# Optimization experiments

Hardware: AMD Instinct MI355X
Metric: run time of the kernel (lower is better)

The kernel has to match this reference:

```python
import jax, jax.numpy as jnp
import numpy as np

N_NODES = 10000
N_EDGES = 160000
NUM_FEAT = 14
DIM = 256


def gat_conv(x, src, dst, W, a_s, a_d, b, concat):
    """PyG GATConv: W [H*C, F_in], a_s/a_d [H, C], edges src->dst (self-loops included)."""
    H, C = a_s.shape
    N = x.shape[0]
    h = (x @ W.T).reshape(N, H, C)                       # [N,H,C]
    alpha_src = (h * a_s).sum(-1)                        # [N,H]
    alpha_dst = (h * a_d).sum(-1)                        # [N,H]
    e = jax.nn.leaky_relu(alpha_src[src] + alpha_dst[dst], negative_slope=0.2)  # [E,H]
    emax = jax.ops.segment_max(e, dst, num_segments=N)   # [N,H]
    emax = jnp.where(jnp.isneginf(emax), 0.0, emax)
    ex = jnp.exp(e - emax[dst])
    denom = jax.ops.segment_sum(ex, dst, num_segments=N)
    coef = ex / (denom[dst] + 1e-16)                     # segment softmax over in-edges
    out = jax.ops.segment_sum(h[src] * coef[..., None], dst, num_segments=N)  # [N,H,C]
    out = out.reshape(N, H * C) if concat else out.mean(axis=1)
    return out + b


def setup_inputs() -> dict:
    key = jax.random.key(0)
    ks = jax.random.split(key, 24)
    d = DIM
    f = NUM_FEAT
    def w(k, shape, fan_in):
        return jax.random.normal(k, shape, dtype=jnp.float32) * (1.0 / np.sqrt(fan_in))
    inp = {
        "x": jax.random.normal(ks[0], (N_NODES, f), dtype=jnp.float32),
        "edge_index": jax.random.randint(ks[1], (2, N_EDGES), 0, N_NODES, dtype=jnp.int64
                                         if jax.config.jax_enable_x64 else jnp.int32),
        # conv1: 14 -> 4 heads x 256
        "W1": w(ks[2], (4 * d, f), f),
        "a1s": w(ks[3], (4, d), d), "a1d": w(ks[4], (4, d), d),
        "b1": jnp.zeros((4 * d,), jnp.float32),
        "lw1": w(ks[5], (4 * d, f), f), "lb1": jnp.zeros((4 * d,), jnp.float32),
        # conv2: 1024 -> 4 heads x 256
        "W2": w(ks[6], (4 * d, 4 * d), 4 * d),
        "a2s": w(ks[7], (4, d), d), "a2d": w(ks[8], (4, d), d),
        "b2": jnp.zeros((4 * d,), jnp.float32),
        "lw2": w(ks[9], (4 * d, 4 * d), 4 * d), "lb2": jnp.zeros((4 * d,), jnp.float32),
        # conv3: 1024 -> 6 heads x 256, mean over heads
        "W3": w(ks[10], (6 * d, 4 * d), 4 * d),
        "a3s": w(ks[11], (6, d), d), "a3d": w(ks[12], (6, d), d),
        "b3": jnp.zeros((d,), jnp.float32),
        "lw3": w(ks[13], (d, 4 * d), 4 * d), "lb3": jnp.zeros((d,), jnp.float32),
    }
    return inp


def reference(x, edge_index, W1, a1s, a1d, b1, lw1, lb1,
              W2, a2s, a2d, b2, lw2, lb2,
              W3, a3s, a3d, b3, lw3, lb3):
    N = x.shape[0]
    loops = jnp.arange(N, dtype=edge_index.dtype)
    src = jnp.concatenate([edge_index[0], loops])
    dst = jnp.concatenate([edge_index[1], loops])
    x1 = jax.nn.elu(gat_conv(x, src, dst, W1, a1s, a1d, b1, True) + x @ lw1.T + lb1)
    x2 = jax.nn.elu(gat_conv(x1, src, dst, W2, a2s, a2d, b2, True) + x1 @ lw2.T + lb2)
    x3 = gat_conv(x2, src, dst, W3, a3s, a3d, b3, False) + x2 @ lw3.T + lb3
    return x3
```

## Files before the change

kernel.cpp:

```cpp
#include <hip/hip_runtime.h>
#include <hip/hip_bf16.h>
#include <cstddef>

#define NN 10000
#define EE0 160000
#define NF 14
#define DC 256

static inline int ceildiv(int a, int b) { return (a + b - 1) / b; }

__device__ __forceinline__ float lrelu02(float x) { return fmaxf(x, 0.2f * x); }

__device__ __forceinline__ short f2bf(float f) {
    unsigned u = __float_as_uint(f);
    unsigned r = (u + 0x7FFFu + ((u >> 16) & 1u)) >> 16;
    return (short)r;
}
__device__ __forceinline__ float bf2f(short s) {
    return __uint_as_float(((unsigned)(unsigned short)s) << 16);
}

typedef __attribute__((ext_vector_type(8))) short bf16x8;
typedef __attribute__((ext_vector_type(4))) float f32x4;

#define GLDS(gaddr, laddr)                                                         \
    __builtin_amdgcn_global_load_lds(                                              \
        (__attribute__((address_space(1))) void*)(gaddr),                          \
        (__attribute__((address_space(3))) void*)(laddr), 16, 0, 0)

__global__ void count_edges_k(const int* __restrict__ ei, int* __restrict__ counts,
                              int E0, int N) {
    int e = blockIdx.x * 256 + threadIdx.x;
    int E = E0 + N;
    if (e >= E) return;
    int dst = (e < E0) ? ei[E0 + e] : (e - E0);
    atomicAdd(&counts[dst], 1);
}

__global__ __launch_bounds__(1024) void scan_k(const int* __restrict__ counts,
                                               int* __restrict__ row_off, int n) {
    __shared__ int sums[1024];
    int t = threadIdx.x;
    int chunk = (n + 1023) >> 10;
    int base = t * chunk;
    int lim = base + chunk; if (lim > n) lim = n;
    int s = 0;
    for (int i = base; i < lim; ++i) s += counts[i];
    sums[t] = s;
    __syncthreads();
    for (int off = 1; off < 1024; off <<= 1) {
        int v = (t >= off) ? sums[t - off] : 0;
        __syncthreads();
        sums[t] += v;
        __syncthreads();
    }
    int run = (t == 0) ? 0 : sums[t - 1];
    for (int i = base; i < lim; ++i) { run += counts[i]; row_off[i + 1] = run; }
    if (t == 0) row_off[0] = 0;
}

__global__ void scatter_k(const int* __restrict__ ei, const int* __restrict__ row_off,
                          int* __restrict__ cursor, int* __restrict__ csr_src,
                          int E0, int N) {
    int e = blockIdx.x * 256 + threadIdx.x;
    int E = E0 + N;
    if (e >= E) return;
    int src, dst;
    if (e < E0) { src = ei[e]; dst = ei[E0 + e]; }
    else        { src = dst = e - E0; }
    int pos = row_off[dst] + atomicAdd(&cursor[dst], 1);
    csr_src[pos] = src;
}

__global__ __launch_bounds__(256) void cvt_bf16_fused_k(
    const float* __restrict__ p0, short* __restrict__ q0, int n0,
    const float* __restrict__ p1, short* __restrict__ q1, int n1,
    const float* __restrict__ p2, short* __restrict__ q2, int n2,
    const float* __restrict__ p3, short* __restrict__ q3, int n3) {
    int i = blockIdx.x * 256 + threadIdx.x;
    const float* in; short* out; int idx;
    if (i < n0) { in = p0; out = q0; idx = i; }
    else if (i < n0 + n1) { in = p1; out = q1; idx = i - n0; }
    else if (i < n0 + n1 + n2) { in = p2; out = q2; idx = i - n0 - n1; }
    else if (i < n0 + n1 + n2 + n3) { in = p3; out = q3; idx = i - n0 - n1 - n2; }
    else return;
    float4 v = ((const float4*)in)[idx];
    short4 o;
    o.x = f2bf(v.x); o.y = f2bf(v.y); o.z = f2bf(v.z); o.w = f2bf(v.w);
    ((short4*)out)[idx] = o;
}

__global__ __launch_bounds__(256) void pad_bf16_k(
    const float* __restrict__ p0, short* __restrict__ q0, int r0,
    const float* __restrict__ p1, short* __restrict__ q1, int r1,
    const float* __restrict__ p2, short* __restrict__ q2, int r2,
    int K, int Kp) {
    int i = blockIdx.x * 256 + threadIdx.x;
    int rows = r0 + r1 + r2;
    int total = rows * Kp;
    if (i >= total) return;
    int row = i / Kp, col = i - row * Kp;
    const float* in; short* out; int r;
    if (row < r0) { in = p0; out = q0; r = row; }
    else if (row < r0 + r1) { in = p1; out = q1; r = row - r0; }
    else { in = p2; out = q2; r = row - r0 - r1; }
    out[(size_t)r * Kp + col] = (col < K) ? f2bf(in[(size_t)r * K + col]) : (short)0;
}

__global__ __launch_bounds__(256) void gemm_bf16_dual(
    const short* __restrict__ A, const short* __restrict__ B,
    const float* __restrict__ b1, const float* __restrict__ b2,
    short* __restrict__ Cb, float* __restrict__ Cf,
    int M, int Nh, int Nf, int K) {
    __shared__ short As[128 * 32];
    __shared__ short Bs[128 * 32];
    const int t = threadIdx.x;
    const int wave = t >> 6, lane = t & 63;
    const int m0 = blockIdx.y * 128, n0 = blockIdx.x * 128;
    const int wm = (wave >> 1) * 64, wn = (wave & 1) * 64;
    const int lane15 = lane & 15, quad = lane >> 4;

    const int lrow = lane >> 2;
    const int lk = ((lane & 3) ^ ((lrow >> 1) & 3)) * 8;
    int arow0 = m0 + wave * 16 + lrow;
    int arow1 = arow0 + 64;
    if (arow0 > M - 1) arow0 = M - 1;
    if (arow1 > M - 1) arow1 = M - 1;
    const short* ag0 = A + (size_t)arow0 * K + lk;
    const short* ag1 = A + (size_t)arow1 * K + lk;
    const short* bg0 = B + (size_t)(n0 + wave * 16 + lrow) * K + lk;
    const short* bg1 = B + (size_t)(n0 + 64 + wave * 16 + lrow) * K + lk;
    short* al0 = &As[(wave * 16) * 32];
    short* al1 = &As[(64 + wave * 16) * 32];
    short* bl0 = &Bs[(wave * 16) * 32];
    short* bl1 = &Bs[(64 + wave * 16) * 32];

    const int rql = (quad ^ ((lane15 >> 1) & 3)) * 8;

    f32x4 acc[4][4];
#pragma unroll
    for (int i = 0; i < 4; ++i)
#pragma unroll
        for (int j = 0; j < 4; ++j) acc[i][j] = (f32x4){0.f, 0.f, 0.f, 0.f};

    for (int k0 = 0; k0 < K; k0 += 32) {
        GLDS(ag0 + k0, al0);
        GLDS(ag1 + k0, al1);
        GLDS(bg0 + k0, bl0);
        GLDS(bg1 + k0, bl1);
        __syncthreads();
        bf16x8 af[4], bfr[4];
#pragma unroll
        for (int i = 0; i < 4; ++i)
            af[i] = *(const bf16x8*)&As[(wm + 16 * i + lane15) * 32 + rql];
#pragma unroll
        for (int j = 0; j < 4; ++j)
            bfr[j] = *(const bf16x8*)&Bs[(wn + 16 * j + lane15) * 32 + rql];
#pragma unroll
        for (int i = 0; i < 4; ++i)
#pragma unroll
            for (int j = 0; j < 4; ++j)
                acc[i][j] = __builtin_amdgcn_mfma_f32_16x16x32_bf16(
                    af[i], bfr[j], acc[i][j], 0, 0, 0);
        __syncthreads();
    }

    if (n0 >= Nh) {
#pragma unroll
        for (int j = 0; j < 4; ++j) {
            int nc = n0 - Nh + wn + 16 * j + lane15;
            float bias = b1[nc] + b2[nc];
#pragma unroll
            for (int i = 0; i < 4; ++i) {
                int mb = m0 + wm + 16 * i + quad * 4;
#pragma unroll
                for (int r = 0; r < 4; ++r) {
                    int m = mb + r;
                    if (m < M) Cf[(size_t)m * Nf + nc] = acc[i][j][r] + bias;
                }
            }
        }
    } else {
#pragma unroll
        for (int j = 0; j < 4; ++j) {
            int n = n0 + wn + 16 * j + lane15;
#pragma unroll
            for (int i = 0; i < 4; ++i) {
                int mb = m0 + wm + 16 * i + quad * 4;
#pragma unroll
                for (int r = 0; r < 4; ++r) {
                    int m = mb + r;
                    if (m < M) Cb[(size_t)m * Nh + n] = f2bf(acc[i][j][r]);
                }
            }
        }
    }
}

__global__ __launch_bounds__(256) void alpha_k(
    const short* __restrict__ h, const float* __restrict__ a_s,
    const float* __restrict__ a_d, float* __restrict__ asrc,
    float* __restrict__ adst, int N, int H) {
    int wid = (int)((blockIdx.x * (size_t)blockDim.x + threadIdx.x) >> 6);
    int lane = threadIdx.x & 63;
    if (wid >= N * H) return;
    int n = wid / H, hh = wid - n * H;
    const short4 hv4 = *(const short4*)(h + (size_t)n * H * DC + hh * DC + lane * 4);
    const float4 sv = *(const float4*)(a_s + hh * DC + lane * 4);
    const float4 dv = *(const float4*)(a_d + hh * DC + lane * 4);
    float hx = bf2f(hv4.x), hy = bf2f(hv4.y), hz = bf2f(hv4.z), hw = bf2f(hv4.w);
    float s = hx * sv.x + hy * sv.y + hz * sv.z + hw * sv.w;
    float d = hx * dv.x + hy * dv.y + hz * dv.z + hw * dv.w;
#pragma unroll
    for (int off = 32; off > 0; off >>= 1) {
        s += __shfl_down(s, off);
        d += __shfl_down(d, off);
    }
    if (lane == 0) { asrc[wid] = s; adst[wid] = d; }
}

__global__ __launch_bounds__(256) void gat_agg(
    const short* __restrict__ hbuf, const float* __restrict__ lin,
    const float* __restrict__ asrc, const float* __restrict__ adst_a,
    const int* __restrict__ row_off, const int* __restrict__ csr_src,
    short* __restrict__ outx, int N, int H) {
    int wid = (int)((blockIdx.x * (size_t)blockDim.x + threadIdx.x) >> 6);
    int lane = threadIdx.x & 63;
    if (wid >= N * H) return;
    int n = wid / H, hh = wid - n * H;
    int beg = row_off[n], end = row_off[n + 1];
    int deg = end - beg;
    float ad = adst_a[wid];

    size_t cbase = (size_t)n * H * DC + hh * DC + lane * 4;
    float4 acc = *(const float4*)(lin + cbase);

    if (deg <= 64) {
        int s = 0; float e = -1e38f;
        if (lane < deg) {
            s = csr_src[beg + lane];
            e = lrelu02(asrc[s * H + hh] + ad);
        }
        float m = e;
#pragma unroll
        for (int off = 32; off > 0; off >>= 1) m = fmaxf(m, __shfl_xor(m, off));
        float p = (lane < deg) ? __expf(e - m) : 0.f;
        float dsum = p;
#pragma unroll
        for (int off = 32; off > 0; off >>= 1) dsum += __shfl_xor(dsum, off);
        float coef = p / (dsum + 1e-16f);

        const size_t hoff = (size_t)hh * DC + lane * 4;
        int i = 0;
        for (; i + 8 <= deg; i += 8) {
            short4 v[8]; float wv[8];
#pragma unroll
            for (int u = 0; u < 8; ++u) {
                int su = __shfl(s, i + u);
                v[u] = *(const short4*)(hbuf + (size_t)su * (H * DC) + hoff);
                wv[u] = __shfl(coef, i + u);
            }
#pragma unroll
            for (int u = 0; u < 8; ++u) {
                acc.x += wv[u] * bf2f(v[u].x);
                acc.y += wv[u] * bf2f(v[u].y);
                acc.z += wv[u] * bf2f(v[u].z);
                acc.w += wv[u] * bf2f(v[u].w);
            }
        }
        for (; i < deg; ++i) {
            float wv = __shfl(coef, i);
            int si = __shfl(s, i);
            const short4 hv = *(const short4*)(hbuf + (size_t)si * (H * DC) + hoff);
            acc.x += wv * bf2f(hv.x); acc.y += wv * bf2f(hv.y);
            acc.z += wv * bf2f(hv.z); acc.w += wv * bf2f(hv.w);
        }
    } else {
        float m = -1e38f;
        for (int i = beg + lane; i < end; i += 64) {
            int s = csr_src[i];
            m = fmaxf(m, lrelu02(asrc[s * H + hh] + ad));
        }
#pragma unroll
        for (int off = 32; off > 0; off >>= 1) m = fmaxf(m, __shfl_xor(m, off));
        float dsum = 0.f;
        for (int i = beg + lane; i < end; i += 64) {
            int s = csr_src[i];
            dsum += __expf(lrelu02(asrc[s * H + hh] + ad) - m);
        }
#pragma unroll
        for (int off = 32; off > 0; off >>= 1) dsum += __shfl_xor(dsum, off);
        float inv = 1.f / (dsum + 1e-16f);
        for (int i = beg; i < end; ++i) {
            int s = csr_src[i];
            float wv = __expf(lrelu02(asrc[s * H + hh] + ad) - m) * inv;
            const short4 hv = *(const short4*)(hbuf + ((size_t)s * H + hh) * DC + lane * 4);
            acc.x += wv * bf2f(hv.x); acc.y += wv * bf2f(hv.y);
            acc.z += wv * bf2f(hv.z); acc.w += wv * bf2f(hv.w);
        }
    }
    acc.x = acc.x > 0.f ? acc.x : __expf(acc.x) - 1.f;
    acc.y = acc.y > 0.f ? acc.y : __expf(acc.y) - 1.f;
    acc.z = acc.z > 0.f ? acc.z : __expf(acc.z) - 1.f;
    acc.w = acc.w > 0.f ? acc.w : __expf(acc.w) - 1.f;
    short4 o;
    o.x = f2bf(acc.x); o.y = f2bf(acc.y); o.z = f2bf(acc.z); o.w = f2bf(acc.w);
    *(short4*)(outx + cbase) = o;
}

__global__ __launch_bounds__(384) void gat_agg_mean(
    const short* __restrict__ hbuf, const float* __restrict__ asrc,
    const float* __restrict__ adst_a, const int* __restrict__ row_off,
    const int* __restrict__ csr_src, float* __restrict__ out, int N) {
    const int H = 6;
    __shared__ float red[6][DC];
    int n = blockIdx.x;
    int wave = threadIdx.x >> 6, lane = threadIdx.x & 63;
    int hh = wave;
    int beg = row_off[n], end = row_off[n + 1];
    int deg = end - beg;
    const float invH = 1.f / 6.f;
    float ad = adst_a[n * H + hh];

    float4 acc = make_float4(0.f, 0.f, 0.f, 0.f);
    const size_t hoff = (size_t)hh * DC + lane * 4;

    if (deg <= 64) {
        int s = 0; float e = -1e38f;
        if (lane < deg) {
            s = csr_src[beg + lane];
            e = lrelu02(asrc[s * H + hh] + ad);
        }
        float m = e;
#pragma unroll
        for (int off = 32; off > 0; off >>= 1) m = fmaxf(m, __shfl_xor(m, off));
        float p = (lane < deg) ? __expf(e - m) : 0.f;
        float dsum = p;
#pragma unroll
        for (int off = 32; off > 0; off >>= 1) dsum += __shfl_xor(dsum, off);
        float coef = p * invH / (dsum + 1e-16f);

        int i = 0;
        for (; i + 8 <= deg; i += 8) {
            short4 v[8]; float wv[8];
#pragma unroll
            for (int u = 0; u < 8; ++u) {
                int su = __shfl(s, i + u);
                v[u] = *(const short4*)(hbuf + (size_t)su * (H * DC) + hoff);
                wv[u] = __shfl(coef, i + u);
            }
#pragma unroll
            for (int u = 0; u < 8; ++u) {
                acc.x += wv[u] * bf2f(v[u].x);
                acc.y += wv[u] * bf2f(v[u].y);
                acc.z += wv[u] * bf2f(v[u].z);
                acc.w += wv[u] * bf2f(v[u].w);
            }
        }
        for (; i < deg; ++i) {
            float wv = __shfl(coef, i);
            int si = __shfl(s, i);
            const short4 hv = *(const short4*)(hbuf + (size_t)si * (H * DC) + hoff);
            acc.x += wv * bf2f(hv.x); acc.y += wv * bf2f(hv.y);
            acc.z += wv * bf2f(hv.z); acc.w += wv * bf2f(hv.w);
        }
    } else {
        float m = -1e38f;
        for (int i = beg + lane; i < end; i += 64) {
            int s = csr_src[i];
            m = fmaxf(m, lrelu02(asrc[s * H + hh] + ad));
        }
#pragma unroll
        for (int off = 32; off > 0; off >>= 1) m = fmaxf(m, __shfl_xor(m, off));
        float dsum = 0.f;
        for (int i = beg + lane; i < end; i += 64) {
            int s = csr_src[i];
            dsum += __expf(lrelu02(asrc[s * H + hh] + ad) - m);
        }
#pragma unroll
        for (int off = 32; off > 0; off >>= 1) dsum += __shfl_xor(dsum, off);
        float inv = invH / (dsum + 1e-16f);
        for (int i = beg; i < end; ++i) {
            int s = csr_src[i];
            float wv = __expf(lrelu02(asrc[s * H + hh] + ad) - m) * inv;
            const short4 hv = *(const short4*)(hbuf + (size_t)s * (H * DC) + hoff);
            acc.x += wv * bf2f(hv.x); acc.y += wv * bf2f(hv.y);
            acc.z += wv * bf2f(hv.z); acc.w += wv * bf2f(hv.w);
        }
    }
    *(float4*)&red[wave][lane * 4] = acc;
    __syncthreads();
    if (wave == 0) {
        float* op = out + (size_t)n * DC + lane * 4;
        float4 o = *(float4*)op;
#pragma unroll
        for (int j = 0; j < 6; ++j) {
            float4 r = *(float4*)&red[j][lane * 4];
            o.x += r.x; o.y += r.y; o.z += r.z; o.w += r.w;
        }
        *(float4*)op = o;
    }
}

extern "C" void kernel_launch(void* const* d_in, const int* in_sizes, int n_in,
                              void* d_out, int out_size, void* d_ws, size_t ws_size,
                              hipStream_t stream) {
    const float* x   = (const float*)d_in[0];
    const int*   ei  = (const int*)d_in[1];
    const float* W1  = (const float*)d_in[2];
    const float* a1s = (const float*)d_in[3];
    const float* a1d = (const float*)d_in[4];
    const float* b1  = (const float*)d_in[5];
    const float* lw1 = (const float*)d_in[6];
    const float* lb1 = (const float*)d_in[7];
    const float* W2  = (const float*)d_in[8];
    const float* a2s = (const float*)d_in[9];
    const float* a2d = (const float*)d_in[10];
    const float* b2  = (const float*)d_in[11];
    const float* lb2_w = (const float*)d_in[12];
    const float* lb2 = (const float*)d_in[13];
    const float* W3  = (const float*)d_in[14];
    const float* a3s = (const float*)d_in[15];
    const float* a3d = (const float*)d_in[16];
    const float* b3  = (const float*)d_in[17];
    const float* lw3 = (const float*)d_in[18];
    const float* lb3 = (const float*)d_in[19];
    const float* lw2 = lb2_w;
    float* out = (float*)d_out;

    const int N = NN, E0 = EE0, E = EE0 + NN;

    unsigned char* w = (unsigned char*)d_ws;
    size_t off = 0;
    auto alloc = [&](size_t bytes) {
        void* p = w + off;
        off += (bytes + 255) & ~(size_t)255;
        return p;
    };
    short* hbuf   = (short*)alloc((size_t)N * 1536 * 2);
    float* buf    = (float*)alloc((size_t)N * 1024 * 4);
    short* xb     = (short*)alloc((size_t)N * 1024 * 2);
    short* xpad   = (short*)alloc((size_t)N * 32 * 2);
    short* W1p    = (short*)alloc((size_t)1024 * 32 * 2);
    short* lw1p   = (short*)alloc((size_t)1024 * 32 * 2);
    short* W2b    = (short*)alloc((size_t)1024 * 1024 * 2);
    short* lw2b   = (short*)alloc((size_t)1024 * 1024 * 2);
    short* W3b    = (short*)alloc((size_t)1536 * 1024 * 2);
    short* lw3b   = (short*)alloc((size_t)256 * 1024 * 2);
    float* asrc   = (float*)alloc((size_t)N * 6 * 4);
    float* adst   = (float*)alloc((size_t)N * 6 * 4);
    int* row_off  = (int*)alloc((size_t)(N + 1) * 4);
    int* counts2  = (int*)alloc((size_t)2 * N * 4);
    int* counts   = counts2;
    int* cursor   = counts2 + N;
    int* csr_src  = (int*)alloc((size_t)E * 4);
    (void)ws_size; (void)n_in; (void)in_sizes; (void)out_size;

    hipMemsetAsync(counts2, 0, (size_t)2 * N * 4, stream);
    count_edges_k<<<ceildiv(E, 256), 256, 0, stream>>>(ei, counts, E0, N);
    scan_k<<<1, 1024, 0, stream>>>(counts, row_off, N);
    scatter_k<<<ceildiv(E, 256), 256, 0, stream>>>(ei, row_off, cursor, csr_src, E0, N);

    {
        int q0 = 1024 * 1024 / 4, q1 = 1024 * 1024 / 4, q2 = 1536 * 1024 / 4,
            q3 = 256 * 1024 / 4;
        cvt_bf16_fused_k<<<ceildiv(q0 + q1 + q2 + q3, 256), 256, 0, stream>>>(
            W2, W2b, q0, lw2, lw2b, q1, W3, W3b, q2, lw3, lw3b, q3);
        int rows = N + 1024 + 1024;
        pad_bf16_k<<<ceildiv(rows * 32, 256), 256, 0, stream>>>(
            x, xpad, N, W1, W1p, 1024, lw1, lw1p, 1024, NF, 32);
    }

    gemm_bf16_dual<<<dim3(16, ceildiv(N, 128)), 256, 0, stream>>>(
        xpad, W1p, b1, lb1, hbuf, buf, N, 1024, 1024, 32);
    alpha_k<<<ceildiv(N * 4, 4), 256, 0, stream>>>(hbuf, a1s, a1d, asrc, adst, N, 4);
    gat_agg<<<ceildiv(N * 4, 4), 256, 0, stream>>>(hbuf, buf, asrc, adst, row_off, csr_src,
                                                   xb, N, 4);

    gemm_bf16_dual<<<dim3(16, ceildiv(N, 128)), 256, 0, stream>>>(
        xb, W2b, b2, lb2, hbuf, buf, N, 1024, 1024, 1024);
    alpha_k<<<ceildiv(N * 4, 4), 256, 0, stream>>>(hbuf, a2s, a2d, asrc, adst, N, 4);
    gat_agg<<<ceildiv(N * 4, 4), 256, 0, stream>>>(hbuf, buf, asrc, adst, row_off, csr_src,
                                                   xb, N, 4);

    gemm_bf16_dual<<<dim3(14, ceildiv(N, 128)), 256, 0, stream>>>(
        xb, W3b, b3, lb3, hbuf, out, N, 1536, 256, 1024);
    alpha_k<<<ceildiv(N * 6, 4), 256, 0, stream>>>(hbuf, a3s, a3d, asrc, adst, N, 6);
    gat_agg_mean<<<N, 384, 0, stream>>>(hbuf, asrc, adst, row_off, csr_src, out, N);
}
```

Baseline: 482.6 us.

## Split each node-head's edge aggregation across two waves with shared-memory softmax reduction

The GAT aggregation kernels now assign two waves to each (node, head) pair. Each wave processes alternating in-edges, and the two combine their softmax max and sum through shared memory and block barriers. The partial feature accumulators are then reduced in LDS before the ELU and store. This doubles the parallelism available to hide gather latency on the memory-bound neighbor loads, at the cost of extra __syncthreads, larger blocks, and LDS traffic. The fast path now covers degrees up to 128.

```diff
diff --git a/kernel.cpp b/kernel.cpp
--- a/kernel.cpp
+++ b/kernel.cpp
@@ -219,40 +219,50 @@
     if (lane == 0) { asrc[wid] = s; adst[wid] = d; }
 }
 
-__global__ __launch_bounds__(256) void gat_agg(
+__global__ __launch_bounds__(512) void gat_agg2(
     const short* __restrict__ hbuf, const float* __restrict__ lin,
     const float* __restrict__ asrc, const float* __restrict__ adst_a,
     const int* __restrict__ row_off, const int* __restrict__ csr_src,
-    short* __restrict__ outx, int N, int H) {
-    int wid = (int)((blockIdx.x * (size_t)blockDim.x + threadIdx.x) >> 6);
-    int lane = threadIdx.x & 63;
-    if (wid >= N * H) return;
-    int n = wid / H, hh = wid - n * H;
+    short* __restrict__ outx, int N) {
+    const int H = 4;
+    __shared__ float smax[8], ssum[8];
+    __shared__ float red[4][DC];
+    int n = blockIdx.x;
+    int wave = threadIdx.x >> 6, lane = threadIdx.x & 63;
+    int head = wave >> 1, half = wave & 1;
     int beg = row_off[n], end = row_off[n + 1];
     int deg = end - beg;
-    float ad = adst_a[wid];
-
-    size_t cbase = (size_t)n * H * DC + hh * DC + lane * 4;
-    float4 acc = *(const float4*)(lin + cbase);
-
-    if (deg <= 64) {
+    float ad = adst_a[n * H + head];
+    const size_t hoff = (size_t)head * DC + lane * 4;
+    const size_t cbase = (size_t)n * (H * DC) + hoff;
+
+    float4 acc;
+    if (half == 0) acc = *(const float4*)(lin + cbase);
+    else           acc = make_float4(0.f, 0.f, 0.f, 0.f);
+
+    if (deg <= 128) {
+        int cnt = (deg - half + 1) >> 1;
         int s = 0; float e = -1e38f;
-        if (lane < deg) {
-            s = csr_src[beg + lane];
-            e = lrelu02(asrc[s * H + hh] + ad);
+        if (lane < cnt) {
+            s = csr_src[beg + half + 2 * lane];
+            e = lrelu02(asrc[s * H + head] + ad);
         }
         float m = e;
 #pragma unroll
         for (int off = 32; off > 0; off >>= 1) m = fmaxf(m, __shfl_xor(m, off));
-        float p = (lane < deg) ? __expf(e - m) : 0.f;
-        float dsum = p;
-#pragma unroll
-        for (int off = 32; off > 0; off >>= 1) dsum += __shfl_xor(dsum, off);
-        float coef = p / (dsum + 1e-16f);
-
-        const size_t hoff = (size_t)hh * DC + lane * 4;
+        if (lane == 0) smax[wave] = m;
+        __syncthreads();
+        m = fmaxf(smax[head * 2], smax[head * 2 + 1]);
+        float p = (lane < cnt) ? __expf(e - m) : 0.f;
+        float ds = p;
+#pragma unroll
+        for (int off = 32; off > 0; off >>= 1) ds += __shfl_xor(ds, off);
+        if (lane == 0) ssum[wave] = ds;
+        __syncthreads();
+        float coef = p / (ssum[head * 2] + ssum[head * 2 + 1] + 1e-16f);
+
         int i = 0;
-        for (; i + 8 <= deg; i += 8) {
+        for (; i + 8 <= cnt; i += 8) {
             short4 v[8]; float wv[8];
 #pragma unroll
             for (int u = 0; u < 8; ++u) {
@@ -268,80 +278,99 @@
                 acc.w += wv[u] * bf2f(v[u].w);
             }
         }
-        for (; i < deg; ++i) {
+        for (; i < cnt; ++i) {
+            int su = __shfl(s, i);
             float wv = __shfl(coef, i);
-            int si = __shfl(s, i);
-            const short4 hv = *(const short4*)(hbuf + (size_t)si * (H * DC) + hoff);
+            const short4 hv = *(const short4*)(hbuf + (size_t)su * (H * DC) + hoff);
             acc.x += wv * bf2f(hv.x); acc.y += wv * bf2f(hv.y);
             acc.z += wv * bf2f(hv.z); acc.w += wv * bf2f(hv.w);
         }
     } else {
         float m = -1e38f;
-        for (int i = beg + lane; i < end; i += 64) {
+        for (int i = beg + half * 64 + lane; i < end; i += 128) {
             int s = csr_src[i];
-            m = fmaxf(m, lrelu02(asrc[s * H + hh] + ad));
+            m = fmaxf(m, lrelu02(asrc[s * H + head] + ad));
         }
 #pragma unroll
         for (int off = 32; off > 0; off >>= 1) m = fmaxf(m, __shfl_xor(m, off));
-        float dsum = 0.f;
-        for (int i = beg + lane; i < end; i += 64) {
+        if (lane == 0) smax[wave] = m;
+        __syncthreads();
+        m = fmaxf(smax[head * 2], smax[head * 2 + 1]);
+        float ds = 0.f;
+        for (int i = beg + half * 64 + lane; i < end; i += 128) {
             int s = csr_src[i];
-            dsum += __expf(lrelu02(asrc[s * H + hh] + ad) - m);
-        }
-#pragma unroll
-        for (int off = 32; off > 0; off >>= 1) dsum += __shfl_xor(dsum, off);
-        float inv = 1.f / (dsum + 1e-16f);
-        for (int i = beg; i < end; ++i) {
+            ds += __expf(lrelu02(asrc[s * H + head] + ad) - m);
+        }
+#pragma unroll
+        for (int off = 32; off > 0; off >>= 1) ds += __shfl_xor(ds, off);
+        if (lane == 0) ssum[wave] = ds;
+        __syncthreads();
+        float inv = 1.f / (ssum[head * 2] + ssum[head * 2 + 1] + 1e-16f);
+        for (int i = beg + half; i < end; i += 2) {
             int s = csr_src[i];
-            float wv = __expf(lrelu02(asrc[s * H + hh] + ad) - m) * inv;
-            const short4 hv = *(const short4*)(hbuf + ((size_t)s * H + hh) * DC + lane * 4);
+            float wv = __expf(lrelu02(asrc[s * H + head] + ad) - m) * inv;
+            const short4 hv = *(const short4*)(hbuf + (size_t)s * (H * DC) + hoff);
             acc.x += wv * bf2f(hv.x); acc.y += wv * bf2f(hv.y);
             acc.z += wv * bf2f(hv.z); acc.w += wv * bf2f(hv.w);
         }
     }
-    acc.x = acc.x > 0.f ? acc.x : __expf(acc.x) - 1.f;
-    acc.y = acc.y > 0.f ? acc.y : __expf(acc.y) - 1.f;
-    acc.z = acc.z > 0.f ? acc.z : __expf(acc.z) - 1.f;
-    acc.w = acc.w > 0.f ? acc.w : __expf(acc.w) - 1.f;
-    short4 o;
-    o.x = f2bf(acc.x); o.y = f2bf(acc.y); o.z = f2bf(acc.z); o.w = f2bf(acc.w);
-    *(short4*)(outx + cbase) = o;
-}
-
-__global__ __launch_bounds__(384) void gat_agg_mean(
+
+    if (half == 1) *(float4*)&red[head][lane * 4] = acc;
+    __syncthreads();
+    if (half == 0) {
+        float4 r = *(float4*)&red[head][lane * 4];
+        acc.x += r.x; acc.y += r.y; acc.z += r.z; acc.w += r.w;
+        acc.x = acc.x > 0.f ? acc.x : __expf(acc.x) - 1.f;
+        acc.y = acc.y > 0.f ? acc.y : __expf(acc.y) - 1.f;
+        acc.z = acc.z > 0.f ? acc.z : __expf(acc.z) - 1.f;
+        acc.w = acc.w > 0.f ? acc.w : __expf(acc.w) - 1.f;
+        short4 o;
+        o.x = f2bf(acc.x); o.y = f2bf(acc.y); o.z = f2bf(acc.z); o.w = f2bf(acc.w);
+        *(short4*)(outx + cbase) = o;
+    }
+}
+
+__global__ __launch_bounds__(768) void gat_agg_mean(
     const short* __restrict__ hbuf, const float* __restrict__ asrc,
     const float* __restrict__ adst_a, const int* __restrict__ row_off,
     const int* __restrict__ csr_src, float* __restrict__ out, int N) {
     const int H = 6;
+    __shared__ float smax[12], ssum[12];
     __shared__ float red[6][DC];
     int n = blockIdx.x;
     int wave = threadIdx.x >> 6, lane = threadIdx.x & 63;
-    int hh = wave;
+    int head = wave >> 1, half = wave & 1;
     int beg = row_off[n], end = row_off[n + 1];
     int deg = end - beg;
     const float invH = 1.f / 6.f;
-    float ad = adst_a[n * H + hh];
+    float ad = adst_a[n * H + head];
+    const size_t hoff = (size_t)head * DC + lane * 4;
 
     float4 acc = make_float4(0.f, 0.f, 0.f, 0.f);
-    const size_t hoff = (size_t)hh * DC + lane * 4;
-
-    if (deg <= 64) {
+
+    if (deg <= 128) {
+        int cnt = (deg - half + 1) >> 1;
         int s = 0; float e = -1e38f;
-        if (lane < deg) {
-            s = csr_src[beg + lane];
-            e = lrelu02(asrc[s * H + hh] + ad);
+        if (lane < cnt) {
+            s = csr_src[beg + half + 2 * lane];
+            e = lrelu02(asrc[s * H + head] + ad);
         }
         float m = e;
 #pragma unroll
         for (int off = 32; off > 0; off >>= 1) m = fmaxf(m, __shfl_xor(m, off));
-        float p = (lane < deg) ? __expf(e - m) : 0.f;
-        float dsum = p;
-#pragma unroll
-        for (int off = 32; off > 0; off >>= 1) dsum += __shfl_xor(dsum, off);
-        float coef = p * invH / (dsum + 1e-16f);
+        if (lane == 0) smax[wave] = m;
+        __syncthreads();
+        m = fmaxf(smax[head * 2], smax[head * 2 + 1]);
+        float p = (lane < cnt) ? __expf(e - m) : 0.f;
+        float ds = p;
+#pragma unroll
+        for (int off = 32; off > 0; off >>= 1) ds += __shfl_xor(ds, off);
+        if (lane == 0) ssum[wave] = ds;
+        __syncthreads();
+        float coef = p * invH / (ssum[head * 2] + ssum[head * 2 + 1] + 1e-16f);
 
         int i = 0;
-        for (; i + 8 <= deg; i += 8) {
+        for (; i + 8 <= cnt; i += 8) {
             short4 v[8]; float wv[8];
 #pragma unroll
             for (int u = 0; u < 8; ++u) {
@@ -357,38 +386,50 @@
                 acc.w += wv[u] * bf2f(v[u].w);
             }
         }
-        for (; i < deg; ++i) {
+        for (; i < cnt; ++i) {
+            int su = __shfl(s, i);
             float wv = __shfl(coef, i);
-            int si = __shfl(s, i);
-            const short4 hv = *(const short4*)(hbuf + (size_t)si * (H * DC) + hoff);
+            const short4 hv = *(const short4*)(hbuf + (size_t)su * (H * DC) + hoff);
             acc.x += wv * bf2f(hv.x); acc.y += wv * bf2f(hv.y);
             acc.z += wv * bf2f(hv.z); acc.w += wv * bf2f(hv.w);
         }
     } else {
         float m = -1e38f;
-        for (int i = beg + lane; i < end; i += 64) {
+        for (int i = beg + half * 64 + lane; i < end; i += 128) {
             int s = csr_src[i];
-            m = fmaxf(m, lrelu02(asrc[s * H + hh] + ad));
+            m = fmaxf(m, lrelu02(asrc[s * H + head] + ad));
         }
 #pragma unroll
         for (int off = 32; off > 0; off >>= 1) m = fmaxf(m, __shfl_xor(m, off));
-        float dsum = 0.f;
-        for (int i = beg + lane; i < end; i += 64) {
+        if (lane == 0) smax[wave] = m;
+        __syncthreads();
+        m = fmaxf(smax[head * 2], smax[head * 2 + 1]);
+        float ds = 0.f;
+        for (int i = beg + half * 64 + lane; i < end; i += 128) {
             int s = csr_src[i];
-            dsum += __expf(lrelu02(asrc[s * H + hh] + ad) - m);
-        }
-#pragma unroll
-        for (int off = 32; off > 0; off >>= 1) dsum += __shfl_xor(dsum, off);
-        float inv = invH / (dsum + 1e-16f);
-        for (int i = beg; i < end; ++i) {
+            ds += __expf(lrelu02(asrc[s * H + head] + ad) - m);
+        }
+#pragma unroll
+        for (int off = 32; off > 0; off >>= 1) ds += __shfl_xor(ds, off);
+        if (lane == 0) ssum[wave] = ds;
+        __syncthreads();
+        float inv = invH / (ssum[head * 2] + ssum[head * 2 + 1] + 1e-16f);
+        for (int i = beg + half; i < end; i += 2) {
             int s = csr_src[i];
-            float wv = __expf(lrelu02(asrc[s * H + hh] + ad) - m) * inv;
+            float wv = __expf(lrelu02(asrc[s * H + head] + ad) - m) * inv;
             const short4 hv = *(const short4*)(hbuf + (size_t)s * (H * DC) + hoff);
             acc.x += wv * bf2f(hv.x); acc.y += wv * bf2f(hv.y);
             acc.z += wv * bf2f(hv.z); acc.w += wv * bf2f(hv.w);
         }
     }
-    *(float4*)&red[wave][lane * 4] = acc;
+
+    if (half == 1) *(float4*)&red[head][lane * 4] = acc;
+    __syncthreads();
+    if (half == 0) {
+        float4 r = *(float4*)&red[head][lane * 4];
+        acc.x += r.x; acc.y += r.y; acc.z += r.z; acc.w += r.w;
+        *(float4*)&red[head][lane * 4] = acc;
+    }
     __syncthreads();
     if (wave == 0) {
         float* op = out + (size_t)n * DC + lane * 4;
@@ -417,7 +458,7 @@
     const float* a2s = (const float*)d_in[9];
     const float* a2d = (const float*)d_in[10];
     const float* b2  = (const float*)d_in[11];
-    const float* lb2_w = (const float*)d_in[12];
+    const float* lw2 = (const float*)d_in[12];
     const float* lb2 = (const float*)d_in[13];
     const float* W3  = (const float*)d_in[14];
     const float* a3s = (const float*)d_in[15];
@@ -425,7 +466,6 @@
     const float* b3  = (const float*)d_in[17];
     const float* lw3 = (const float*)d_in[18];
     const float* lb3 = (const float*)d_in[19];
-    const float* lw2 = lb2_w;
     float* out = (float*)d_out;
 
     const int N = NN, E0 = EE0, E = EE0 + NN;
@@ -474,17 +514,15 @@
     gemm_bf16_dual<<<dim3(16, ceildiv(N, 128)), 256, 0, stream>>>(
         xpad, W1p, b1, lb1, hbuf, buf, N, 1024, 1024, 32);
     alpha_k<<<ceildiv(N * 4, 4), 256, 0, stream>>>(hbuf, a1s, a1d, asrc, adst, N, 4);
-    gat_agg<<<ceildiv(N * 4, 4), 256, 0, stream>>>(hbuf, buf, asrc, adst, row_off, csr_src,
-                                                   xb, N, 4);
+    gat_agg2<<<N, 512, 0, stream>>>(hbuf, buf, asrc, adst, row_off, csr_src, xb, N);
 
     gemm_bf16_dual<<<dim3(16, ceildiv(N, 128)), 256, 0, stream>>>(
         xb, W2b, b2, lb2, hbuf, buf, N, 1024, 1024, 1024);
     alpha_k<<<ceildiv(N * 4, 4), 256, 0, stream>>>(hbuf, a2s, a2d, asrc, adst, N, 4);
-    gat_agg<<<ceildiv(N * 4, 4), 256, 0, stream>>>(hbuf, buf, asrc, adst, row_off, csr_src,
-                                                   xb, N, 4);
+    gat_agg2<<<N, 512, 0, stream>>>(hbuf, buf, asrc, adst, row_off, csr_src, xb, N);
 
     gemm_bf16_dual<<<dim3(14, ceildiv(N, 128)), 256, 0, stream>>>(
         xb, W3b, b3, lb3, hbuf, out, N, 1536, 256, 1024);
     alpha_k<<<ceildiv(N * 6, 4), 256, 0, stream>>>(hbuf, a3s, a3d, asrc, adst, N, 6);
-    gat_agg_mean<<<N, 384, 0, stream>>>(hbuf, asrc, adst, row_off, csr_src, out, N);
-}
+    gat_agg_mean<<<N, 768, 0, stream>>>(hbuf, asrc, adst, row_off, csr_src, out, N);
+}
```

Result: slower. 526.5 us (+9.1%).

## Fold attention vectors into weights and fuse alpha into aggregation epilogue

Applied to the files above, without the earlier changes.

Precomputes per-head projections a^T W for each layer so attention logits become dot products with the layer input instead of the bf16 output h. Layer-1 logits are computed directly from x, and layers 2/3 logits are computed in the gat_agg epilogue from the freshly produced activations. This removes three alpha_k passes that reread hbuf. In exchange it adds a small weight-vector kernel and extra per-node reductions plus a block barrier in gat_agg, and the logits now come from full-precision weights applied to bf16 inputs rather than from bf16-rounded h.

```diff
diff --git a/kernel.cpp b/kernel.cpp
--- a/kernel.cpp
+++ b/kernel.cpp
@@ -107,6 +107,59 @@
     out[(size_t)r * Kp + col] = (col < K) ? f2bf(in[(size_t)r * K + col]) : (short)0;
 }
 
+__global__ __launch_bounds__(256) void wv_k(
+    const float* __restrict__ W1, const float* __restrict__ a1s, const float* __restrict__ a1d,
+    const float* __restrict__ W2, const float* __restrict__ a2s, const float* __restrict__ a2d,
+    const float* __restrict__ W3, const float* __restrict__ a3s, const float* __restrict__ a3d,
+    float* __restrict__ wv1, float* __restrict__ wv2, float* __restrict__ wv3) {
+    int i = blockIdx.x * 256 + threadIdx.x;
+    if (i < 8 * 1024) {
+        int o = i >> 10, k = i & 1023;
+        int h = o >> 1;
+        const float* av = (o & 1) ? a2d : a2s;
+        float acc = 0.f;
+        for (int c = 0; c < 256; ++c)
+            acc += av[h * 256 + c] * W2[(size_t)(h * 256 + c) * 1024 + k];
+        wv2[o * 1024 + k] = acc;
+    } else if (i < 8 * 1024 + 12 * 1024) {
+        int j = i - 8 * 1024;
+        int o = j >> 10, k = j & 1023;
+        int h = o >> 1;
+        const float* av = (o & 1) ? a3d : a3s;
+        float acc = 0.f;
+        for (int c = 0; c < 256; ++c)
+            acc += av[h * 256 + c] * W3[(size_t)(h * 256 + c) * 1024 + k];
+        wv3[o * 1024 + k] = acc;
+    } else if (i < 8 * 1024 + 12 * 1024 + 8 * 16) {
+        int j = i - 8 * 1024 - 12 * 1024;
+        int o = j >> 4, k = j & 15;
+        int h = o >> 1;
+        float acc = 0.f;
+        if (k < NF) {
+            const float* av = (o & 1) ? a1d : a1s;
+            for (int c = 0; c < 256; ++c)
+                acc += av[h * 256 + c] * W1[(size_t)(h * 256 + c) * NF + k];
+        }
+        wv1[o * 16 + k] = acc;
+    }
+}
+
+__global__ __launch_bounds__(256) void alpha1_k(
+    const float* __restrict__ x, const float* __restrict__ wv1,
+    float* __restrict__ asrc, float* __restrict__ adst, int N) {
+    int i = blockIdx.x * 256 + threadIdx.x;
+    if (i >= N * 8) return;
+    int n = i >> 3, o = i & 7;
+    const float* xr = x + (size_t)n * NF;
+    const float* wr = wv1 + o * 16;
+    float s = 0.f;
+#pragma unroll
+    for (int k = 0; k < NF; ++k) s += xr[k] * wr[k];
+    int h = o >> 1;
+    if (o & 1) adst[n * 4 + h] = s;
+    else       asrc[n * 4 + h] = s;
+}
+
 __global__ __launch_bounds__(256) void gemm_bf16_dual(
     const short* __restrict__ A, const short* __restrict__ B,
     const float* __restrict__ b1, const float* __restrict__ b2,
@@ -197,40 +250,20 @@
     }
 }
 
-__global__ __launch_bounds__(256) void alpha_k(
-    const short* __restrict__ h, const float* __restrict__ a_s,
-    const float* __restrict__ a_d, float* __restrict__ asrc,
-    float* __restrict__ adst, int N, int H) {
-    int wid = (int)((blockIdx.x * (size_t)blockDim.x + threadIdx.x) >> 6);
-    int lane = threadIdx.x & 63;
-    if (wid >= N * H) return;
-    int n = wid / H, hh = wid - n * H;
-    const short4 hv4 = *(const short4*)(h + (size_t)n * H * DC + hh * DC + lane * 4);
-    const float4 sv = *(const float4*)(a_s + hh * DC + lane * 4);
-    const float4 dv = *(const float4*)(a_d + hh * DC + lane * 4);
-    float hx = bf2f(hv4.x), hy = bf2f(hv4.y), hz = bf2f(hv4.z), hw = bf2f(hv4.w);
-    float s = hx * sv.x + hy * sv.y + hz * sv.z + hw * sv.w;
-    float d = hx * dv.x + hy * dv.y + hz * dv.z + hw * dv.w;
-#pragma unroll
-    for (int off = 32; off > 0; off >>= 1) {
-        s += __shfl_down(s, off);
-        d += __shfl_down(d, off);
-    }
-    if (lane == 0) { asrc[wid] = s; adst[wid] = d; }
-}
-
 __global__ __launch_bounds__(256) void gat_agg(
     const short* __restrict__ hbuf, const float* __restrict__ lin,
     const float* __restrict__ asrc, const float* __restrict__ adst_a,
     const int* __restrict__ row_off, const int* __restrict__ csr_src,
-    short* __restrict__ outx, int N, int H) {
-    int wid = (int)((blockIdx.x * (size_t)blockDim.x + threadIdx.x) >> 6);
-    int lane = threadIdx.x & 63;
-    if (wid >= N * H) return;
-    int n = wid / H, hh = wid - n * H;
+    short* __restrict__ outx, const float* __restrict__ wvn,
+    float* __restrict__ asrc_n, float* __restrict__ adst_n,
+    int N, int n_out) {
+    const int H = 4;
+    __shared__ float sred[4][12];
+    int n = blockIdx.x;
+    int hh = threadIdx.x >> 6, lane = threadIdx.x & 63;
     int beg = row_off[n], end = row_off[n + 1];
     int deg = end - beg;
-    float ad = adst_a[wid];
+    float ad = adst_a[n * H + hh];
 
     size_t cbase = (size_t)n * H * DC + hh * DC + lane * 4;
     float4 acc = *(const float4*)(lin + cbase);
@@ -306,6 +339,25 @@
     short4 o;
     o.x = f2bf(acc.x); o.y = f2bf(acc.y); o.z = f2bf(acc.z); o.w = f2bf(acc.w);
     *(short4*)(outx + cbase) = o;
+
+    float r0 = bf2f(o.x), r1 = bf2f(o.y), r2 = bf2f(o.z), r3 = bf2f(o.w);
+    const float* wbase = wvn + hh * DC + lane * 4;
+    for (int k = 0; k < n_out; ++k) {
+        const float* wr = wbase + k * 1024;
+        float p = r0 * wr[0] + r1 * wr[1] + r2 * wr[2] + r3 * wr[3];
+#pragma unroll
+        for (int off = 32; off > 0; off >>= 1) p += __shfl_xor(p, off);
+        if (lane == 0) sred[hh][k] = p;
+    }
+    __syncthreads();
+    if (threadIdx.x < (unsigned)n_out) {
+        int k = threadIdx.x;
+        float sum = sred[0][k] + sred[1][k] + sred[2][k] + sred[3][k];
+        int h2 = k >> 1;
+        int H2 = n_out >> 1;
+        if (k & 1) adst_n[n * H2 + h2] = sum;
+        else       asrc_n[n * H2 + h2] = sum;
+    }
 }
 
 __global__ __launch_bounds__(384) void gat_agg_mean(
@@ -417,7 +469,7 @@
     const float* a2s = (const float*)d_in[9];
     const float* a2d = (const float*)d_in[10];
     const float* b2  = (const float*)d_in[11];
-    const float* lb2_w = (const float*)d_in[12];
+    const float* lw2 = (const float*)d_in[12];
     const float* lb2 = (const float*)d_in[13];
     const float* W3  = (const float*)d_in[14];
     const float* a3s = (const float*)d_in[15];
@@ -425,7 +477,6 @@
     const float* b3  = (const float*)d_in[17];
     const float* lw3 = (const float*)d_in[18];
     const float* lb3 = (const float*)d_in[19];
-    const float* lw2 = lb2_w;
     float* out = (float*)d_out;
 
     const int N = NN, E0 = EE0, E = EE0 + NN;
@@ -447,8 +498,15 @@
     short* lw2b   = (short*)alloc((size_t)1024 * 1024 * 2);
     short* W3b    = (short*)alloc((size_t)1536 * 1024 * 2);
     short* lw3b   = (short*)alloc((size_t)256 * 1024 * 2);
-    float* asrc   = (float*)alloc((size_t)N * 6 * 4);
-    float* adst   = (float*)alloc((size_t)N * 6 * 4);
+    float* asrc1  = (float*)alloc((size_t)N * 4 * 4);
+    float* adst1  = (float*)alloc((size_t)N * 4 * 4);
+    float* asrc2  = (float*)alloc((size_t)N * 4 * 4);
+    float* adst2  = (float*)alloc((size_t)N * 4 * 4);
+    float* asrc3  = (float*)alloc((size_t)N * 6 * 4);
+    float* adst3  = (float*)alloc((size_t)N * 6 * 4);
+    float* wv1    = (float*)alloc((size_t)8 * 16 * 4);
+    float* wv2    = (float*)alloc((size_t)8 * 1024 * 4);
+    float* wv3    = (float*)alloc((size_t)12 * 1024 * 4);
     int* row_off  = (int*)alloc((size_t)(N + 1) * 4);
     int* counts2  = (int*)alloc((size_t)2 * N * 4);
     int* counts   = counts2;
@@ -469,22 +527,22 @@
         int rows = N + 1024 + 1024;
         pad_bf16_k<<<ceildiv(rows * 32, 256), 256, 0, stream>>>(
             x, xpad, N, W1, W1p, 1024, lw1, lw1p, 1024, NF, 32);
+        wv_k<<<ceildiv(8 * 1024 + 12 * 1024 + 8 * 16, 256), 256, 0, stream>>>(
+            W1, a1s, a1d, W2, a2s, a2d, W3, a3s, a3d, wv1, wv2, wv3);
+        alpha1_k<<<ceildiv(N * 8, 256), 256, 0, stream>>>(x, wv1, asrc1, adst1, N);
     }
 
     gemm_bf16_dual<<<dim3(16, ceildiv(N, 128)), 256, 0, stream>>>(
         xpad, W1p, b1, lb1, hbuf, buf, N, 1024, 1024, 32);
-    alpha_k<<<ceildiv(N * 4, 4), 256, 0, stream>>>(hbuf, a1s, a1d, asrc, adst, N, 4);
-    gat_agg<<<ceildiv(N * 4, 4), 256, 0, stream>>>(hbuf, buf, asrc, adst, row_off, csr_src,
-                                                   xb, N, 4);
+    gat_agg<<<N, 256, 0, stream>>>(hbuf, buf, asrc1, adst1, row_off, csr_src,
+                                   xb, wv2, asrc2, adst2, N, 8);
 
     gemm_bf16_dual<<<dim3(16, ceildiv(N, 128)), 256, 0, stream>>>(
         xb, W2b, b2, lb2, hbuf, buf, N, 1024, 1024, 1024);
-    alpha_k<<<ceildiv(N * 4, 4), 256, 0, stream>>>(hbuf, a2s, a2d, asrc, adst, N, 4);
-    gat_agg<<<ceildiv(N * 4, 4), 256, 0, stream>>>(hbuf, buf, asrc, adst, row_off, csr_src,
-                                                   xb, N, 4);
+    gat_agg<<<N, 256, 0, stream>>>(hbuf, buf, asrc2, adst2, row_off, csr_src,
+                                   xb, wv3, asrc3, adst3, N, 12);
 
     gemm_bf16_dual<<<dim3(14, ceildiv(N, 128)), 256, 0, stream>>>(
         xb, W3b, b3, lb3, hbuf, out, N, 1536, 256, 1024);
-    alpha_k<<<ceildiv(N * 6, 4), 256, 0, stream>>>(hbuf, a3s, a3d, asrc, adst, N, 6);
-    gat_agg_mean<<<N, 384, 0, stream>>>(hbuf, asrc, adst, row_off, csr_src, out, N);
-}
+    gat_agg_mean<<<N, 384, 0, stream>>>(hbuf, asrc3, adst3, row_off, csr_src, out, N);
+}
```

After: 514.4 us. 1.07x slower.
